# Optimization experiments

Measured on AMD Instinct MI355X. Metric: run time of the kernel, lower is better.

## Reference

```python
import jax, jax.numpy as jnp
import numpy as np

D_MODEL = 1024
N_HEADS = 16
D_K = D_MODEL // N_HEADS
TEMP = 0.01
THRESH = 0.019
NEG_INF = -1e9


def setup_inputs() -> dict:
    key = jax.random.key(0)
    ks = jax.random.split(key, 10)
    B, S = 4, 1024
    # xavier_uniform gain=1 for square [D,D]: limit = sqrt(6/(D+D))
    lim_w = float(np.sqrt(6.0 / (D_MODEL + D_MODEL)))
    # nn.Linear default bias init: U(-1/sqrt(fan_in), 1/sqrt(fan_in))
    lim_b = float(1.0 / np.sqrt(D_MODEL))
    return {
        "user_ID": jax.random.randint(ks[0], (B,), 0, 100000),
        "Q": jax.random.normal(ks[1], (B, S, D_MODEL), jnp.float32),
        "K": jax.random.normal(ks[2], (B, S, D_MODEL), jnp.float32),
        "V": jax.random.normal(ks[3], (B, S, D_MODEL), jnp.float32),
        "Wq": jax.random.uniform(ks[4], (D_MODEL, D_MODEL), jnp.float32, -lim_w, lim_w),
        "bq": jax.random.uniform(ks[5], (D_MODEL,), jnp.float32, -lim_b, lim_b),
        "Wk": jax.random.uniform(ks[6], (D_MODEL, D_MODEL), jnp.float32, -lim_w, lim_w),
        "bk": jax.random.uniform(ks[7], (D_MODEL,), jnp.float32, -lim_b, lim_b),
        "Wv": jax.random.uniform(ks[8], (D_MODEL, D_MODEL), jnp.float32, -lim_w, lim_w),
        "bv": jax.random.uniform(ks[9], (D_MODEL,), jnp.float32, -lim_b, lim_b),
    }


def _split_heads(x):
    B, S, _ = x.shape
    return x.reshape(B, S, N_HEADS, D_K).transpose(0, 2, 1, 3)  # [B,H,S,Dk]


def reference(user_ID, Q, K, V, Wq, bq, Wk, bk, Wv, bv):
    # nn.Linear: y = x @ W.T + b
    q = _split_heads(Q @ Wq.T + bq)
    k = _split_heads(K @ Wk.T + bk)
    v = _split_heads(V @ Wv.T + bv)
    scores = jnp.einsum("bhqd,bhkd->bhqk", q, k) / jnp.sqrt(jnp.float32(D_K))
    # temperature-sharpened softmax used only to build the sparse mask
    attn_sharp = jax.nn.softmax(scores / TEMP, axis=-1)
    mask_sparse = attn_sharp < THRESH
    scores = jnp.where(mask_sparse, jnp.float32(NEG_INF), scores)
    attn = jax.nn.softmax(scores, axis=-1)
    ctx = jnp.einsum("bhqk,bhkd->bhqd", attn, v)
    B, H, S, Dk = ctx.shape
    return ctx.transpose(0, 2, 1, 3).reshape(B, S, H * Dk)
```

## Files before the change

kernel.cpp:

```cpp
#include <hip/hip_runtime.h>

constexpr int D = 1024;
constexpr int S = 1024;
constexpr int NB = 4;
constexpr int NH = 16;
constexpr int DK = 64;
constexpr float THRESH = 0.019f;
constexpr int ROWS = 8;
constexpr int SSP = 1056;

typedef __attribute__((ext_vector_type(8))) short bf16x8;
typedef __attribute__((ext_vector_type(4))) float f32x4;

__device__ __forceinline__ float wave_max(float v) {
#pragma unroll
    for (int off = 32; off >= 1; off >>= 1)
        v = fmaxf(v, __shfl_xor(v, off, 64));
    return v;
}
__device__ __forceinline__ float wave_sum(float v) {
#pragma unroll
    for (int off = 32; off >= 1; off >>= 1)
        v += __shfl_xor(v, off, 64);
    return v;
}

__device__ __forceinline__ int cvtpk(float lo, float hi) {
    int r;
    asm("v_cvt_pk_bf16_f32 %0, %1, %2" : "=v"(r) : "v"(lo), "v"(hi));
    return r;
}
__device__ __forceinline__ bf16x8 pack_bf8(float4 a, float4 b) {
    union { int i[4]; bf16x8 v; } u;
    u.i[0] = cvtpk(a.x, a.y);
    u.i[1] = cvtpk(a.z, a.w);
    u.i[2] = cvtpk(b.x, b.y);
    u.i[3] = cvtpk(b.z, b.w);
    return u.v;
}

__global__ __launch_bounds__(256) void proj_kernel(
    const float* __restrict__ Qi, const float* __restrict__ Ki, const float* __restrict__ Vi,
    const float* __restrict__ Wq, const float* __restrict__ bq,
    const float* __restrict__ Wk, const float* __restrict__ bk,
    const float* __restrict__ Wv, const float* __restrict__ bv,
    float* __restrict__ qo, float* __restrict__ ko, float* __restrict__ vo)
{
    const int pz = blockIdx.z;
    const float* __restrict__ X    = (pz == 0) ? Qi : (pz == 1) ? Ki : Vi;
    const float* __restrict__ W    = (pz == 0) ? Wq : (pz == 1) ? Wk : Wv;
    const float* __restrict__ bias = (pz == 0) ? bq : (pz == 1) ? bk : bv;
    float* __restrict__ out        = (pz == 0) ? qo : (pz == 1) ? ko : vo;

    __shared__ __align__(16) float Xs[2][16][132];
    __shared__ __align__(16) float Ws[2][16][132];

    const int t  = threadIdx.x;
    const int tx = t & 15;
    const int ty = t >> 4;
    const int m0 = blockIdx.y * 128;
    const int n0 = blockIdx.x * 128;
    const int lr = t >> 1;
    const int lc = (t & 1) << 3;

    const float* __restrict__ Xp = X + (size_t)(m0 + lr) * D + lc;
    const float* __restrict__ Wp = W + (size_t)(n0 + lr) * D + lc;

    float4 xa = *(const float4*)(Xp + 0);
    float4 xb = *(const float4*)(Xp + 4);
    float4 wa = *(const float4*)(Wp + 0);
    float4 wb = *(const float4*)(Wp + 4);
    Xs[0][lc + 0][lr] = xa.x; Xs[0][lc + 1][lr] = xa.y; Xs[0][lc + 2][lr] = xa.z; Xs[0][lc + 3][lr] = xa.w;
    Xs[0][lc + 4][lr] = xb.x; Xs[0][lc + 5][lr] = xb.y; Xs[0][lc + 6][lr] = xb.z; Xs[0][lc + 7][lr] = xb.w;
    Ws[0][lc + 0][lr] = wa.x; Ws[0][lc + 1][lr] = wa.y; Ws[0][lc + 2][lr] = wa.z; Ws[0][lc + 3][lr] = wa.w;
    Ws[0][lc + 4][lr] = wb.x; Ws[0][lc + 5][lr] = wb.y; Ws[0][lc + 6][lr] = wb.z; Ws[0][lc + 7][lr] = wb.w;
    __syncthreads();

    float acc[8][8] = {};
    int buf = 0;

    for (int k0 = 0; k0 < D; k0 += 16) {
        const bool more = (k0 + 16) < D;
        if (more) {
            xa = *(const float4*)(Xp + k0 + 16);
            xb = *(const float4*)(Xp + k0 + 20);
            wa = *(const float4*)(Wp + k0 + 16);
            wb = *(const float4*)(Wp + k0 + 20);
        }
#pragma unroll
        for (int kk = 0; kk < 16; ++kk) {
            float4 a0 = *(const float4*)&Xs[buf][kk][(ty << 2)];
            float4 a1 = *(const float4*)&Xs[buf][kk][64 + (ty << 2)];
            float4 b0 = *(const float4*)&Ws[buf][kk][(tx << 2)];
            float4 b1 = *(const float4*)&Ws[buf][kk][64 + (tx << 2)];
            float av[8]  = {a0.x, a0.y, a0.z, a0.w, a1.x, a1.y, a1.z, a1.w};
            float bv8[8] = {b0.x, b0.y, b0.z, b0.w, b1.x, b1.y, b1.z, b1.w};
#pragma unroll
            for (int i = 0; i < 8; ++i)
#pragma unroll
                for (int j = 0; j < 8; ++j)
                    acc[i][j] += av[i] * bv8[j];
        }
        if (more) {
            const int nb = buf ^ 1;
            Xs[nb][lc + 0][lr] = xa.x; Xs[nb][lc + 1][lr] = xa.y; Xs[nb][lc + 2][lr] = xa.z; Xs[nb][lc + 3][lr] = xa.w;
            Xs[nb][lc + 4][lr] = xb.x; Xs[nb][lc + 5][lr] = xb.y; Xs[nb][lc + 6][lr] = xb.z; Xs[nb][lc + 7][lr] = xb.w;
            Ws[nb][lc + 0][lr] = wa.x; Ws[nb][lc + 1][lr] = wa.y; Ws[nb][lc + 2][lr] = wa.z; Ws[nb][lc + 3][lr] = wa.w;
            Ws[nb][lc + 4][lr] = wb.x; Ws[nb][lc + 5][lr] = wb.y; Ws[nb][lc + 6][lr] = wb.z; Ws[nb][lc + 7][lr] = wb.w;
            __syncthreads();
            buf = nb;
        }
    }

    const int bb2 = m0 >> 10;
    if (pz == 1) {
        const int s_base = (m0 & 1023) + (ty << 2);
#pragma unroll
        for (int g = 0; g < 2; ++g) {
            const int hh = (n0 >> 6) + g;
#pragma unroll
            for (int jj = 0; jj < 4; ++jj) {
                const int d = (tx << 2) + jj;
                const int j = (g << 2) + jj;
                const float bj = bias[n0 + (g << 6) + d];
                float* op = &out[(((size_t)bb2 * NH + hh) * DK + d) * S];
                *(float4*)(op + s_base) =
                    make_float4(acc[0][j] + bj, acc[1][j] + bj, acc[2][j] + bj, acc[3][j] + bj);
                *(float4*)(op + s_base + 64) =
                    make_float4(acc[4][j] + bj, acc[5][j] + bj, acc[6][j] + bj, acc[7][j] + bj);
            }
        }
    } else {
        float bj[8];
#pragma unroll
        for (int j = 0; j < 8; ++j)
            bj[j] = bias[n0 + ((j >> 2) << 6) + (tx << 2) + (j & 3)];
#pragma unroll
        for (int i = 0; i < 8; ++i) {
            const int sr = (m0 & 1023) + ((i >> 2) << 6) + (ty << 2) + (i & 3);
#pragma unroll
            for (int g = 0; g < 2; ++g) {
                const int hh = (n0 >> 6) + g;
                float* op = &out[(((size_t)bb2 * NH + hh) * S + sr) * DK + (tx << 2)];
                *(float4*)op = make_float4(acc[i][(g << 2) + 0] + bj[(g << 2) + 0],
                                           acc[i][(g << 2) + 1] + bj[(g << 2) + 1],
                                           acc[i][(g << 2) + 2] + bj[(g << 2) + 2],
                                           acc[i][(g << 2) + 3] + bj[(g << 2) + 3]);
            }
        }
    }
}

__global__ __launch_bounds__(256) void attn_kernel(
    const float* __restrict__ qw, const float* __restrict__ kw,
    const float* __restrict__ vw, float* __restrict__ out)
{
    __shared__ __align__(16) float ss[ROWS][SSP];
    __shared__ __align__(16) float qT[DK][ROWS];
    __shared__ float rowinv[ROWS];

    const int t    = threadIdx.x;
    const int lane = t & 63;
    const int w    = t >> 6;

    const int L   = blockIdx.x + (S / ROWS) * (blockIdx.y + NH * blockIdx.z);
    const int swz = (L & 7) * ((S / ROWS) * NH * NB / 8) + (L >> 3);
    const int qx  = swz & (S / ROWS - 1);
    const int h   = (swz >> 7) & (NH - 1);
    const int b   = swz >> 11;

    const size_t base = ((size_t)b * NH + h) * S * DK;
    const float* __restrict__ qp = qw + base;
    const float* __restrict__ kp = kw + base;
    const float* __restrict__ vp = vw + base;
    const int q0 = qx * ROWS;

#pragma unroll
    for (int p = 0; p < 2; ++p) {
        int e = t + 256 * p;
        int d = e >> 3, r = e & 7;
        qT[d][r] = qp[(size_t)(q0 + r) * DK + d] * 0.125f;
    }
    __syncthreads();

    float accf[ROWS][4] = {};
    const float* __restrict__ kTb = kp + 4 * t;

    float4 kbuf[4];
#pragma unroll
    for (int d = 0; d < 4; ++d)
        kbuf[d] = *(const float4*)&kTb[(size_t)d * S];

#pragma unroll
    for (int d0 = 0; d0 < DK; d0 += 4) {
        float4 kc[4] = {kbuf[0], kbuf[1], kbuf[2], kbuf[3]};
        if (d0 < DK - 4) {
#pragma unroll
            for (int d = 0; d < 4; ++d)
                kbuf[d] = *(const float4*)&kTb[(size_t)(d0 + 4 + d) * S];
        }
#pragma unroll
        for (int dd = 0; dd < 4; ++dd) {
            const int d = d0 + dd;
            float4 qa = *(const float4*)&qT[d][0];
            float4 qb = *(const float4*)&qT[d][4];
            float qr[8] = {qa.x, qa.y, qa.z, qa.w, qb.x, qb.y, qb.z, qb.w};
            float k4[4] = {kc[dd].x, kc[dd].y, kc[dd].z, kc[dd].w};
#pragma unroll
            for (int r = 0; r < ROWS; ++r)
#pragma unroll
                for (int i = 0; i < 4; ++i)
                    accf[r][i] += qr[r] * k4[i];
        }
    }
#pragma unroll
    for (int r = 0; r < ROWS; ++r)
        *(float4*)&ss[r][4 * t] = make_float4(accf[r][0], accf[r][1], accf[r][2], accf[r][3]);
    __syncthreads();

    for (int rr = w; rr < ROWS; rr += 4) {
        float mx = -3.4e38f;
#pragma unroll
        for (int p = 0; p < S / 64; ++p)
            mx = fmaxf(mx, ss[rr][lane + 64 * p]);
        mx = wave_max(mx);

        float zs = 0.f;
#pragma unroll
        for (int p = 0; p < S / 64; ++p)
            zs += __expf(100.f * (ss[rr][lane + 64 * p] - mx));
        zs = wave_sum(zs);

        const bool any = !((1.0f / zs) < THRESH);

        float z2 = 0.f;
#pragma unroll
        for (int p = 0; p < S / 64; ++p) {
            float x = ss[rr][lane + 64 * p];
            float e = __expf(100.f * (x - mx));
            bool keep = !((e / zs) < THRESH);
            float e2 = any ? (keep ? __expf(x - mx) : 0.f) : 1.f;
            z2 += e2;
            ss[rr][lane + 64 * p] = e2;
        }
        z2 = wave_sum(z2);
        if (lane == 0) rowinv[rr] = 1.0f / z2;
    }
    __syncthreads();

    {
        const int cr = lane & 15;
        const int gq = lane >> 4;
        const float* __restrict__ vB = vp + (size_t)(gq * 8) * DK + (w * 16 + cr);
        const float* __restrict__ arow = &ss[lane & 7][gq * 8];

        float bnx[8];
#pragma unroll
        for (int jj = 0; jj < 8; ++jj) bnx[jj] = vB[(size_t)jj * DK];

        f32x4 acc4 = {0.f, 0.f, 0.f, 0.f};
#pragma unroll 4
        for (int ks = 0; ks < 32; ++ks) {
            float bcur[8];
#pragma unroll
            for (int jj = 0; jj < 8; ++jj) bcur[jj] = bnx[jj];
            if (ks < 31) {
#pragma unroll
                for (int jj = 0; jj < 8; ++jj)
                    bnx[jj] = vB[(size_t)((ks + 1) * 32 + jj) * DK];
            }
            float4 a0 = *(const float4*)&arow[ks * 32];
            float4 a1 = *(const float4*)&arow[ks * 32 + 4];
            bf16x8 af = pack_bf8(a0, a1);
            bf16x8 bf = pack_bf8(make_float4(bcur[0], bcur[1], bcur[2], bcur[3]),
                                 make_float4(bcur[4], bcur[5], bcur[6], bcur[7]));
            acc4 = __builtin_amdgcn_mfma_f32_16x16x32_bf16(af, bf, acc4, 0, 0, 0);
        }

        if (gq < 2) {
            const int dcol = h * DK + w * 16 + cr;
#pragma unroll
            for (int reg = 0; reg < 4; ++reg) {
                const int r = gq * 4 + reg;
                out[((size_t)b * S + q0 + r) * D + dcol] = acc4[reg] * rowinv[r];
            }
        }
    }
}

extern "C" void kernel_launch(void* const* d_in, const int* in_sizes, int n_in,
                              void* d_out, int out_size, void* d_ws, size_t ws_size,
                              hipStream_t stream) {
    const float* Qi = (const float*)d_in[1];
    const float* Ki = (const float*)d_in[2];
    const float* Vi = (const float*)d_in[3];
    const float* Wq = (const float*)d_in[4];
    const float* bq = (const float*)d_in[5];
    const float* Wk = (const float*)d_in[6];
    const float* bk = (const float*)d_in[7];
    const float* Wv = (const float*)d_in[8];
    const float* bv = (const float*)d_in[9];
    float* outp = (float*)d_out;

    float* qws = (float*)d_ws;
    float* kws = qws + (size_t)NB * NH * S * DK;
    float* vws = kws + (size_t)NB * NH * S * DK;

    dim3 g1(D / 128, (NB * S) / 128, 3);
    proj_kernel<<<g1, 256, 0, stream>>>(Qi, Ki, Vi, Wq, bq, Wk, bk, Wv, bv, qws, kws, vws);

    dim3 g2(S / ROWS, NH, NB);
    attn_kernel<<<g2, 256, 0, stream>>>(qws, kws, vws, outp);
}
```

Before: 603.1 us.

## Compute V projection with bf16 MFMA inside fused projection kernel

The projection kernel now runs as a flat grid. Blocks 0-511 do the Q and K projections with the existing fp32 FMA tiling, and blocks 512-767 compute the V projection by converting tiles to bf16 in shared memory and using 16x16x32 bf16 MFMA instructions. The shared memory is a union so both paths fit in one kernel. The attention score buffer padding also changes from 1056 to 1044. The aim is to cut the FP32 ALU time of the V GEMM, at the cost of bf16 rounding in V and uneven work across block types.

```diff
diff --git a/kernel.cpp b/kernel.cpp
--- a/kernel.cpp
+++ b/kernel.cpp
@@ -7,7 +7,7 @@
 constexpr int DK = 64;
 constexpr float THRESH = 0.019f;
 constexpr int ROWS = 8;
-constexpr int SSP = 1056;
+constexpr int SSP = 1044;
 
 typedef __attribute__((ext_vector_type(8))) short bf16x8;
 typedef __attribute__((ext_vector_type(4))) float f32x4;
@@ -39,113 +39,196 @@
     return u.v;
 }
 
-__global__ __launch_bounds__(256) void proj_kernel(
+__global__ __launch_bounds__(256) void proj_fused(
     const float* __restrict__ Qi, const float* __restrict__ Ki, const float* __restrict__ Vi,
     const float* __restrict__ Wq, const float* __restrict__ bq,
     const float* __restrict__ Wk, const float* __restrict__ bk,
     const float* __restrict__ Wv, const float* __restrict__ bv,
     float* __restrict__ qo, float* __restrict__ ko, float* __restrict__ vo)
 {
-    const int pz = blockIdx.z;
-    const float* __restrict__ X    = (pz == 0) ? Qi : (pz == 1) ? Ki : Vi;
-    const float* __restrict__ W    = (pz == 0) ? Wq : (pz == 1) ? Wk : Wv;
-    const float* __restrict__ bias = (pz == 0) ? bq : (pz == 1) ? bk : bv;
-    float* __restrict__ out        = (pz == 0) ? qo : (pz == 1) ? ko : vo;
-
-    __shared__ __align__(16) float Xs[2][16][132];
-    __shared__ __align__(16) float Ws[2][16][132];
-
-    const int t  = threadIdx.x;
-    const int tx = t & 15;
-    const int ty = t >> 4;
-    const int m0 = blockIdx.y * 128;
-    const int n0 = blockIdx.x * 128;
-    const int lr = t >> 1;
-    const int lc = (t & 1) << 3;
-
-    const float* __restrict__ Xp = X + (size_t)(m0 + lr) * D + lc;
-    const float* __restrict__ Wp = W + (size_t)(n0 + lr) * D + lc;
-
-    float4 xa = *(const float4*)(Xp + 0);
-    float4 xb = *(const float4*)(Xp + 4);
-    float4 wa = *(const float4*)(Wp + 0);
-    float4 wb = *(const float4*)(Wp + 4);
-    Xs[0][lc + 0][lr] = xa.x; Xs[0][lc + 1][lr] = xa.y; Xs[0][lc + 2][lr] = xa.z; Xs[0][lc + 3][lr] = xa.w;
-    Xs[0][lc + 4][lr] = xb.x; Xs[0][lc + 5][lr] = xb.y; Xs[0][lc + 6][lr] = xb.z; Xs[0][lc + 7][lr] = xb.w;
-    Ws[0][lc + 0][lr] = wa.x; Ws[0][lc + 1][lr] = wa.y; Ws[0][lc + 2][lr] = wa.z; Ws[0][lc + 3][lr] = wa.w;
-    Ws[0][lc + 4][lr] = wb.x; Ws[0][lc + 5][lr] = wb.y; Ws[0][lc + 6][lr] = wb.z; Ws[0][lc + 7][lr] = wb.w;
-    __syncthreads();
-
-    float acc[8][8] = {};
-    int buf = 0;
-
-    for (int k0 = 0; k0 < D; k0 += 16) {
-        const bool more = (k0 + 16) < D;
-        if (more) {
-            xa = *(const float4*)(Xp + k0 + 16);
-            xb = *(const float4*)(Xp + k0 + 20);
-            wa = *(const float4*)(Wp + k0 + 16);
-            wb = *(const float4*)(Wp + k0 + 20);
-        }
-#pragma unroll
-        for (int kk = 0; kk < 16; ++kk) {
-            float4 a0 = *(const float4*)&Xs[buf][kk][(ty << 2)];
-            float4 a1 = *(const float4*)&Xs[buf][kk][64 + (ty << 2)];
-            float4 b0 = *(const float4*)&Ws[buf][kk][(tx << 2)];
-            float4 b1 = *(const float4*)&Ws[buf][kk][64 + (tx << 2)];
-            float av[8]  = {a0.x, a0.y, a0.z, a0.w, a1.x, a1.y, a1.z, a1.w};
-            float bv8[8] = {b0.x, b0.y, b0.z, b0.w, b1.x, b1.y, b1.z, b1.w};
-#pragma unroll
-            for (int i = 0; i < 8; ++i)
-#pragma unroll
-                for (int j = 0; j < 8; ++j)
-                    acc[i][j] += av[i] * bv8[j];
-        }
-        if (more) {
-            const int nb = buf ^ 1;
-            Xs[nb][lc + 0][lr] = xa.x; Xs[nb][lc + 1][lr] = xa.y; Xs[nb][lc + 2][lr] = xa.z; Xs[nb][lc + 3][lr] = xa.w;
-            Xs[nb][lc + 4][lr] = xb.x; Xs[nb][lc + 5][lr] = xb.y; Xs[nb][lc + 6][lr] = xb.z; Xs[nb][lc + 7][lr] = xb.w;
-            Ws[nb][lc + 0][lr] = wa.x; Ws[nb][lc + 1][lr] = wa.y; Ws[nb][lc + 2][lr] = wa.z; Ws[nb][lc + 3][lr] = wa.w;
-            Ws[nb][lc + 4][lr] = wb.x; Ws[nb][lc + 5][lr] = wb.y; Ws[nb][lc + 6][lr] = wb.z; Ws[nb][lc + 7][lr] = wb.w;
-            __syncthreads();
-            buf = nb;
-        }
-    }
-
-    const int bb2 = m0 >> 10;
-    if (pz == 1) {
-        const int s_base = (m0 & 1023) + (ty << 2);
-#pragma unroll
-        for (int g = 0; g < 2; ++g) {
-            const int hh = (n0 >> 6) + g;
-#pragma unroll
-            for (int jj = 0; jj < 4; ++jj) {
-                const int d = (tx << 2) + jj;
-                const int j = (g << 2) + jj;
-                const float bj = bias[n0 + (g << 6) + d];
-                float* op = &out[(((size_t)bb2 * NH + hh) * DK + d) * S];
-                *(float4*)(op + s_base) =
-                    make_float4(acc[0][j] + bj, acc[1][j] + bj, acc[2][j] + bj, acc[3][j] + bj);
-                *(float4*)(op + s_base + 64) =
-                    make_float4(acc[4][j] + bj, acc[5][j] + bj, acc[6][j] + bj, acc[7][j] + bj);
-            }
-        }
-    } else {
-        float bj[8];
-#pragma unroll
-        for (int j = 0; j < 8; ++j)
-            bj[j] = bias[n0 + ((j >> 2) << 6) + (tx << 2) + (j & 3)];
-#pragma unroll
-        for (int i = 0; i < 8; ++i) {
-            const int sr = (m0 & 1023) + ((i >> 2) << 6) + (ty << 2) + (i & 3);
+    __shared__ __align__(16) union SM {
+        struct { float Xs[2][16][132]; float Ws[2][16][132]; } f;
+        struct { short Ah[128][40];    short Bh[128][40];    } v;
+    } sm;
+
+    const int bid = blockIdx.x;
+    const int t   = threadIdx.x;
+
+    if (bid < 512) {
+        const int pz = bid >> 8;
+        const int rb = bid & 255;
+        const int n0 = (rb & 7) * 128;
+        const int m0 = (rb >> 3) * 128;
+
+        const float* __restrict__ X    = (pz == 0) ? Qi : Ki;
+        const float* __restrict__ W    = (pz == 0) ? Wq : Wk;
+        const float* __restrict__ bias = (pz == 0) ? bq : bk;
+
+        const int tx = t & 15;
+        const int ty = t >> 4;
+        const int lr = t >> 1;
+        const int lc = (t & 1) << 3;
+
+        const float* __restrict__ Xp = X + (size_t)(m0 + lr) * D + lc;
+        const float* __restrict__ Wp = W + (size_t)(n0 + lr) * D + lc;
+
+        float4 xa = *(const float4*)(Xp + 0);
+        float4 xb = *(const float4*)(Xp + 4);
+        float4 wa = *(const float4*)(Wp + 0);
+        float4 wb = *(const float4*)(Wp + 4);
+        sm.f.Xs[0][lc + 0][lr] = xa.x; sm.f.Xs[0][lc + 1][lr] = xa.y; sm.f.Xs[0][lc + 2][lr] = xa.z; sm.f.Xs[0][lc + 3][lr] = xa.w;
+        sm.f.Xs[0][lc + 4][lr] = xb.x; sm.f.Xs[0][lc + 5][lr] = xb.y; sm.f.Xs[0][lc + 6][lr] = xb.z; sm.f.Xs[0][lc + 7][lr] = xb.w;
+        sm.f.Ws[0][lc + 0][lr] = wa.x; sm.f.Ws[0][lc + 1][lr] = wa.y; sm.f.Ws[0][lc + 2][lr] = wa.z; sm.f.Ws[0][lc + 3][lr] = wa.w;
+        sm.f.Ws[0][lc + 4][lr] = wb.x; sm.f.Ws[0][lc + 5][lr] = wb.y; sm.f.Ws[0][lc + 6][lr] = wb.z; sm.f.Ws[0][lc + 7][lr] = wb.w;
+        __syncthreads();
+
+        float acc[8][8] = {};
+        int buf = 0;
+
+        for (int k0 = 0; k0 < D; k0 += 16) {
+            const bool more = (k0 + 16) < D;
+            if (more) {
+                xa = *(const float4*)(Xp + k0 + 16);
+                xb = *(const float4*)(Xp + k0 + 20);
+                wa = *(const float4*)(Wp + k0 + 16);
+                wb = *(const float4*)(Wp + k0 + 20);
+            }
+#pragma unroll
+            for (int kk = 0; kk < 16; ++kk) {
+                float4 a0 = *(const float4*)&sm.f.Xs[buf][kk][(ty << 2)];
+                float4 a1 = *(const float4*)&sm.f.Xs[buf][kk][64 + (ty << 2)];
+                float4 b0 = *(const float4*)&sm.f.Ws[buf][kk][(tx << 2)];
+                float4 b1 = *(const float4*)&sm.f.Ws[buf][kk][64 + (tx << 2)];
+                float av[8]  = {a0.x, a0.y, a0.z, a0.w, a1.x, a1.y, a1.z, a1.w};
+                float bv8[8] = {b0.x, b0.y, b0.z, b0.w, b1.x, b1.y, b1.z, b1.w};
+#pragma unroll
+                for (int i = 0; i < 8; ++i)
+#pragma unroll
+                    for (int j = 0; j < 8; ++j)
+                        acc[i][j] += av[i] * bv8[j];
+            }
+            if (more) {
+                const int nb = buf ^ 1;
+                sm.f.Xs[nb][lc + 0][lr] = xa.x; sm.f.Xs[nb][lc + 1][lr] = xa.y; sm.f.Xs[nb][lc + 2][lr] = xa.z; sm.f.Xs[nb][lc + 3][lr] = xa.w;
+                sm.f.Xs[nb][lc + 4][lr] = xb.x; sm.f.Xs[nb][lc + 5][lr] = xb.y; sm.f.Xs[nb][lc + 6][lr] = xb.z; sm.f.Xs[nb][lc + 7][lr] = xb.w;
+                sm.f.Ws[nb][lc + 0][lr] = wa.x; sm.f.Ws[nb][lc + 1][lr] = wa.y; sm.f.Ws[nb][lc + 2][lr] = wa.z; sm.f.Ws[nb][lc + 3][lr] = wa.w;
+                sm.f.Ws[nb][lc + 4][lr] = wb.x; sm.f.Ws[nb][lc + 5][lr] = wb.y; sm.f.Ws[nb][lc + 6][lr] = wb.z; sm.f.Ws[nb][lc + 7][lr] = wb.w;
+                __syncthreads();
+                buf = nb;
+            }
+        }
+
+        const int bb2 = m0 >> 10;
+        if (pz == 1) {
+            const int s_base = (m0 & 1023) + (ty << 2);
 #pragma unroll
             for (int g = 0; g < 2; ++g) {
                 const int hh = (n0 >> 6) + g;
-                float* op = &out[(((size_t)bb2 * NH + hh) * S + sr) * DK + (tx << 2)];
-                *(float4*)op = make_float4(acc[i][(g << 2) + 0] + bj[(g << 2) + 0],
-                                           acc[i][(g << 2) + 1] + bj[(g << 2) + 1],
-                                           acc[i][(g << 2) + 2] + bj[(g << 2) + 2],
-                                           acc[i][(g << 2) + 3] + bj[(g << 2) + 3]);
+#pragma unroll
+                for (int jj = 0; jj < 4; ++jj) {
+                    const int d = (tx << 2) + jj;
+                    const int j = (g << 2) + jj;
+                    const float bj = bias[n0 + (g << 6) + d];
+                    float* op = &ko[(((size_t)bb2 * NH + hh) * DK + d) * S];
+                    *(float4*)(op + s_base) =
+                        make_float4(acc[0][j] + bj, acc[1][j] + bj, acc[2][j] + bj, acc[3][j] + bj);
+                    *(float4*)(op + s_base + 64) =
+                        make_float4(acc[4][j] + bj, acc[5][j] + bj, acc[6][j] + bj, acc[7][j] + bj);
+                }
+            }
+        } else {
+            float bj[8];
+#pragma unroll
+            for (int j = 0; j < 8; ++j)
+                bj[j] = bias[n0 + ((j >> 2) << 6) + (tx << 2) + (j & 3)];
+#pragma unroll
+            for (int i = 0; i < 8; ++i) {
+                const int sr = (m0 & 1023) + ((i >> 2) << 6) + (ty << 2) + (i & 3);
+#pragma unroll
+                for (int g = 0; g < 2; ++g) {
+                    const int hh = (n0 >> 6) + g;
+                    float* op = &qo[(((size_t)bb2 * NH + hh) * S + sr) * DK + (tx << 2)];
+                    *(float4*)op = make_float4(acc[i][(g << 2) + 0] + bj[(g << 2) + 0],
+                                               acc[i][(g << 2) + 1] + bj[(g << 2) + 1],
+                                               acc[i][(g << 2) + 2] + bj[(g << 2) + 2],
+                                               acc[i][(g << 2) + 3] + bj[(g << 2) + 3]);
+                }
+            }
+        }
+    } else {
+        const int vix = bid - 512;
+        const int n0 = (vix & 7) * 128;
+        const int m0 = (vix >> 3) * 128;
+        const int lane = t & 63;
+        const int w4 = t >> 6;
+        const int wm = w4 >> 1;
+        const int wn = w4 & 1;
+        const int cr = lane & 15;
+        const int gq = lane >> 4;
+        const int ar = t >> 1;
+        const int ha = (t & 1) * 16;
+
+        const float* __restrict__ Ap = Vi + (size_t)(m0 + ar) * D + ha;
+        const float* __restrict__ Bp = Wv + (size_t)(n0 + ar) * D + ha;
+
+        float4 a0 = *(const float4*)(Ap + 0), a1 = *(const float4*)(Ap + 4);
+        float4 a2 = *(const float4*)(Ap + 8), a3 = *(const float4*)(Ap + 12);
+        float4 b0 = *(const float4*)(Bp + 0), b1 = *(const float4*)(Bp + 4);
+        float4 b2 = *(const float4*)(Bp + 8), b3 = *(const float4*)(Bp + 12);
+
+        f32x4 acc[4][4];
+#pragma unroll
+        for (int mi = 0; mi < 4; ++mi)
+#pragma unroll
+            for (int nj = 0; nj < 4; ++nj)
+                acc[mi][nj] = (f32x4){0.f, 0.f, 0.f, 0.f};
+
+        for (int ks = 0; ks < 32; ++ks) {
+            *(int4*)&sm.v.Ah[ar][ha + 0] = make_int4(cvtpk(a0.x, a0.y), cvtpk(a0.z, a0.w),
+                                                     cvtpk(a1.x, a1.y), cvtpk(a1.z, a1.w));
+            *(int4*)&sm.v.Ah[ar][ha + 8] = make_int4(cvtpk(a2.x, a2.y), cvtpk(a2.z, a2.w),
+                                                     cvtpk(a3.x, a3.y), cvtpk(a3.z, a3.w));
+            *(int4*)&sm.v.Bh[ar][ha + 0] = make_int4(cvtpk(b0.x, b0.y), cvtpk(b0.z, b0.w),
+                                                     cvtpk(b1.x, b1.y), cvtpk(b1.z, b1.w));
+            *(int4*)&sm.v.Bh[ar][ha + 8] = make_int4(cvtpk(b2.x, b2.y), cvtpk(b2.z, b2.w),
+                                                     cvtpk(b3.x, b3.y), cvtpk(b3.z, b3.w));
+            __syncthreads();
+            if (ks < 31) {
+                a0 = *(const float4*)(Ap + (ks + 1) * 32 + 0);
+                a1 = *(const float4*)(Ap + (ks + 1) * 32 + 4);
+                a2 = *(const float4*)(Ap + (ks + 1) * 32 + 8);
+                a3 = *(const float4*)(Ap + (ks + 1) * 32 + 12);
+                b0 = *(const float4*)(Bp + (ks + 1) * 32 + 0);
+                b1 = *(const float4*)(Bp + (ks + 1) * 32 + 4);
+                b2 = *(const float4*)(Bp + (ks + 1) * 32 + 8);
+                b3 = *(const float4*)(Bp + (ks + 1) * 32 + 12);
+            }
+            bf16x8 af[4];
+#pragma unroll
+            for (int mi = 0; mi < 4; ++mi)
+                af[mi] = *(const bf16x8*)&sm.v.Ah[64 * wm + 16 * mi + cr][gq * 8];
+#pragma unroll
+            for (int nj = 0; nj < 4; ++nj) {
+                bf16x8 bf = *(const bf16x8*)&sm.v.Bh[64 * wn + 16 * nj + cr][gq * 8];
+#pragma unroll
+                for (int mi = 0; mi < 4; ++mi)
+                    acc[mi][nj] = __builtin_amdgcn_mfma_f32_16x16x32_bf16(af[mi], bf, acc[mi][nj], 0, 0, 0);
+            }
+            __syncthreads();
+        }
+
+        const int bb = m0 >> 10;
+#pragma unroll
+        for (int nj = 0; nj < 4; ++nj) {
+            const int n = n0 + 64 * wn + 16 * nj + cr;
+            const float bj = bv[n];
+            const int hh = n >> 6, dk = n & 63;
+#pragma unroll
+            for (int mi = 0; mi < 4; ++mi) {
+                const int s0 = (m0 & 1023) + 64 * wm + 16 * mi + gq * 4;
+#pragma unroll
+                for (int reg = 0; reg < 4; ++reg)
+                    vo[(((size_t)bb * NH + hh) * S + s0 + reg) * DK + dk] = acc[mi][nj][reg] + bj;
             }
         }
     }
@@ -306,8 +389,8 @@
     float* kws = qws + (size_t)NB * NH * S * DK;
     float* vws = kws + (size_t)NB * NH * S * DK;
 
-    dim3 g1(D / 128, (NB * S) / 128, 3);
-    proj_kernel<<<g1, 256, 0, stream>>>(Qi, Ki, Vi, Wq, bq, Wk, bk, Wv, bv, qws, kws, vws);
+    proj_fused<<<dim3(768), 256, 0, stream>>>(Qi, Ki, Vi, Wq, bq, Wk, bk, Wv, bv,
+                                              qws, kws, vws);
 
     dim3 g2(S / ROWS, NH, NB);
     attn_kernel<<<g2, 256, 0, stream>>>(qws, kws, vws, outp);
```

Result: faster. 580.6 us (-3.7%).
